# Optimization experiments

Hardware: AMD Instinct MI355X
Metric: run time of the kernel (lower is better)

Reference implementation:

```python
import jax, jax.numpy as jnp
import numpy as np

D_MODEL = 512
N_HEADS = 8
HEAD_DIM = D_MODEL // N_HEADS
NEG_INF = -1e9


def setup_inputs() -> dict:
    key = jax.random.key(0)
    ks = jax.random.split(key, 12)
    B, N, M = 8, 2048, 2048
    inp = {
        'query': jax.random.normal(ks[0], (B, D_MODEL, N), jnp.float32),
        'key': jax.random.normal(ks[1], (B, D_MODEL, M), jnp.float32),
        'value': jax.random.normal(ks[2], (B, D_MODEL, M), jnp.float32),
        'query_mask': jnp.ones((B, N), jnp.float32),
        'key_value_mask': jnp.ones((B, M), jnp.float32),
        # Conv1d(d_model, d_model, kernel_size=1) == pointwise linear: W [out, in], b [out]
        'Wq': jax.random.normal(ks[3], (D_MODEL, D_MODEL), jnp.float32) / np.sqrt(D_MODEL),
        'bq': jax.random.normal(ks[4], (D_MODEL,), jnp.float32) * 0.01,
        'Wk': jax.random.normal(ks[5], (D_MODEL, D_MODEL), jnp.float32) / np.sqrt(D_MODEL),
        'bk': jax.random.normal(ks[6], (D_MODEL,), jnp.float32) * 0.01,
        'Wv': jax.random.normal(ks[7], (D_MODEL, D_MODEL), jnp.float32) / np.sqrt(D_MODEL),
        'bv': jax.random.normal(ks[8], (D_MODEL,), jnp.float32) * 0.01,
        'Wm': jax.random.normal(ks[9], (D_MODEL, D_MODEL), jnp.float32) / np.sqrt(D_MODEL),
        'bm': jax.random.normal(ks[10], (D_MODEL,), jnp.float32) * 0.01,
    }
    return inp


def _pointwise(W, b, x):
    # Conv1d k=1 over [B, C_in, N] -> [B, C_out, N]
    return jnp.einsum('oi,bin->bon', W, x) + b[None, :, None]


def reference(query, key, value, query_mask, key_value_mask,
              Wq, bq, Wk, bk, Wv, bv, Wm, bm):
    B = query.shape[0]
    N = query.shape[2]
    M = key.shape[2]
    # project and split heads: [B, head_dim, n_heads, seq]
    q = _pointwise(Wq, bq, query).reshape(B, HEAD_DIM, N_HEADS, N)
    k = _pointwise(Wk, bk, key).reshape(B, HEAD_DIM, N_HEADS, M)
    v = _pointwise(Wv, bv, value).reshape(B, HEAD_DIM, N_HEADS, M)
    # scores [B, H, N, M], scaled by sqrt(head_dim) (query.shape[1] post-split)
    scores = jnp.einsum('bdhn,bdhm->bhnm', q, k) / jnp.sqrt(jnp.float32(HEAD_DIM))
    # dual mask: outer product of key_value_mask [B,1,1,M] and query_mask [B,1,N,1]
    mask = key_value_mask[:, None, None, :] * query_mask[:, None, :, None]
    scores = jnp.where(mask > 0, scores, NEG_INF)
    prob = jax.nn.softmax(scores, axis=-1)  # [B, H, N, M]
    x = jnp.einsum('bhnm,bdhm->bdhn', prob, v)  # [B, head_dim, H, N]
    out = _pointwise(Wm, bm, x.reshape(B, D_MODEL, N))
    return out
```

## Files before the change

### kernel.cpp

```cpp
#include <hip/hip_runtime.h>


typedef _Float16 f16;
typedef _Float16 f16x4 __attribute__((ext_vector_type(4)));
typedef _Float16 f16x8 __attribute__((ext_vector_type(8)));
typedef float f32x4 __attribute__((ext_vector_type(4)));

#define D_MODEL 512
#define HD 64
#define SEQ 2048
#define QSCL 0.18033688011112042f
#define KVNEG -1.4426950409e9f
#define FMAXB -6.0f

__global__ __launch_bounds__(256) void k_transpose(
    const float* __restrict__ q, const float* __restrict__ k, const float* __restrict__ v,
    f16* __restrict__ XT)
{
  __shared__ __align__(16) f16 Ts[64][72];
  int t = threadIdx.x;
  int nt = blockIdx.x, ct = blockIdx.y, z = blockIdx.z;
  int src = z >> 3, b = z & 7;
  const float* S = (src == 0) ? q : (src == 1) ? k : v;
  {
    int cr = t >> 2, ns = t & 3;
    const float* p = S + ((size_t)b * D_MODEL + ct * 64 + cr) * SEQ + nt * 64 + ns * 16;
    f32x4 a0 = *(const f32x4*)(p);
    f32x4 a1 = *(const f32x4*)(p + 4);
    f32x4 a2 = *(const f32x4*)(p + 8);
    f32x4 a3 = *(const f32x4*)(p + 12);
    f16x8 h0, h1;
#pragma unroll
    for (int j = 0; j < 4; ++j) { h0[j] = (f16)a0[j]; h0[4 + j] = (f16)a1[j]; h1[j] = (f16)a2[j]; h1[4 + j] = (f16)a3[j]; }
    *(f16x8*)&Ts[cr][ns * 16] = h0;
    *(f16x8*)&Ts[cr][ns * 16 + 8] = h1;
  }
  __syncthreads();
  {
    int nr = t >> 2, cs = t & 3;
    f16x8 h0, h1;
#pragma unroll
    for (int j = 0; j < 8; ++j) h0[j] = Ts[cs * 16 + j][nr];
#pragma unroll
    for (int j = 0; j < 8; ++j) h1[j] = Ts[cs * 16 + 8 + j][nr];
    f16* dst = XT + (((size_t)z) * SEQ + nt * 64 + nr) * D_MODEL + ct * 64 + cs * 16;
    *(f16x8*)dst = h0;
    *(f16x8*)(dst + 8) = h1;
  }
}

__global__ __launch_bounds__(256) void k_wconv(
    const float* __restrict__ Wq, const float* __restrict__ Wk, const float* __restrict__ Wv,
    const float* __restrict__ Wm, f16* __restrict__ W3, f16* __restrict__ Wmh)
{
  int idx = blockIdx.x * 256 + threadIdx.x;
  if (idx < 262144) {
    W3[idx] = (f16)Wq[idx];
    W3[262144 + idx] = (f16)Wk[idx];
    W3[524288 + idx] = (f16)Wv[idx];
    int o = idx >> 9, c = idx & 511;
    int h = c & 7, d = c >> 3;
    Wmh[((size_t)h * 512 + o) * 64 + d] = (f16)Wm[idx];
  }
}

__global__ __launch_bounds__(256, 2) void k_proj(
    const f16* __restrict__ W3, const float* __restrict__ bq, const float* __restrict__ bk,
    const float* __restrict__ bv, const f16* __restrict__ XT,
    f16* __restrict__ Qt, f16* __restrict__ Kt, f16* __restrict__ Vh)
{
  __shared__ __align__(16) char smem[36864];
  f16 (*As)[72] = (f16(*)[72])smem;
  f16 (*Bs)[72] = (f16(*)[72])(smem + 18432);
  f16 (*Ls)[136] = (f16(*)[136])smem;

  int t = threadIdx.x;
  int proj = blockIdx.z, b = blockIdx.y;
  int ot = blockIdx.x & 3, ntile = blockIdx.x >> 2;
  int w = t >> 6, ln = t & 63, i16 = ln & 15, q4 = ln >> 4;
  int ow = w >> 1, nw = w & 1;

  const f16* Wp = W3 + (size_t)proj * 262144;
  const f16* Xp = XT + ((size_t)proj * 8 + b) * (size_t)SEQ * D_MODEL;

  f32x4 acc[4][4];
#pragma unroll
  for (int x = 0; x < 4; ++x)
#pragma unroll
    for (int y = 0; y < 4; ++y) acc[x][y] = (f32x4){0.f, 0.f, 0.f, 0.f};

  int srow = t >> 1, shalf = t & 1;
  for (int kc = 0; kc < 8; ++kc) {
    __syncthreads();
    const f16* Ap = Wp + ((size_t)(ot * 128 + srow)) * 512 + kc * 64 + shalf * 32;
#pragma unroll
    for (int s8 = 0; s8 < 4; ++s8)
      *(f32x4*)&As[srow][shalf * 32 + s8 * 8] = *(const f32x4*)(Ap + s8 * 8);
    const f16* Bp = Xp + ((size_t)(ntile * 128 + srow)) * 512 + kc * 64 + shalf * 32;
#pragma unroll
    for (int s8 = 0; s8 < 4; ++s8)
      *(f32x4*)&Bs[srow][shalf * 32 + s8 * 8] = *(const f32x4*)(Bp + s8 * 8);
    __syncthreads();
#pragma unroll
    for (int kk = 0; kk < 2; ++kk) {
      f16x8 af[4], bf[4];
#pragma unroll
      for (int x = 0; x < 4; ++x) af[x] = *(const f16x8*)&As[ow * 64 + x * 16 + i16][kk * 32 + q4 * 8];
#pragma unroll
      for (int y = 0; y < 4; ++y) bf[y] = *(const f16x8*)&Bs[nw * 64 + y * 16 + i16][kk * 32 + q4 * 8];
#pragma unroll
      for (int x = 0; x < 4; ++x)
#pragma unroll
        for (int y = 0; y < 4; ++y)
          acc[x][y] = __builtin_amdgcn_mfma_f32_16x16x32_f16(af[x], bf[y], acc[x][y], 0, 0, 0);
    }
  }

  const float* bias = (proj == 0) ? bq : (proj == 1) ? bk : bv;
  float scl = (proj == 0) ? QSCL : 1.0f;
  __syncthreads();
#pragma unroll
  for (int x = 0; x < 4; ++x) {
    f32x4 bb = *(const f32x4*)(bias + ot * 128 + ow * 64 + x * 16 + q4 * 4);
#pragma unroll
    for (int y = 0; y < 4; ++y)
#pragma unroll
      for (int r = 0; r < 4; ++r)
        Ls[ow * 64 + x * 16 + q4 * 4 + r][nw * 64 + y * 16 + i16] = (f16)((acc[x][y][r] + bb[r]) * scl);
  }
  __syncthreads();
  if (proj < 2) {
    f16* dst = (proj == 0) ? Qt : Kt;
    int n = t >> 1, seg = t & 1;
#pragma unroll
    for (int h = 0; h < 8; ++h) {
      f16x8 g;
#pragma unroll
      for (int j = 0; j < 8; ++j) g[j] = Ls[8 * (seg * 8 + j) + h][n];
      f16* dp = dst + (((size_t)((b * 8 + h) * 4 + ot)) * 2048 + ntile * 128 + n) * 16 + seg * 8;
      *(f16x8*)dp = g;
    }
  } else {
#pragma unroll
    for (int p = 0; p < 8; ++p) {
      int ol = (t >> 4) + 16 * p;
      int ch = t & 15;
      int og = ot * 128 + ol;
      int h = og & 7, d = og >> 3;
      f16* dp = Vh + (((size_t)(b * 8 + h)) * HD + d) * SEQ + ntile * 128 + ch * 8;
      *(f32x4*)dp = *(const f32x4*)&Ls[ol][ch * 8];
    }
  }
}

__global__ __launch_bounds__(256, 4) void k_attn(
    const f16* __restrict__ Qt, const f16* __restrict__ Kt, const f16* __restrict__ Vh,
    const float* __restrict__ qmask, const float* __restrict__ kvmask,
    f16* __restrict__ O)
{
  __shared__ __align__(16) char smem[18432];
  f16 (*Qs)[72] = (f16(*)[72])smem;
  f16 (*Ks)[72] = (f16(*)[72])smem;
  f16 (*Vs)[72] = (f16(*)[72])(smem + 9216);

  int t = threadIdx.x;
  int bh = blockIdx.x >> 4;
  int b = bh >> 3;
  int n0 = (blockIdx.x & 15) * 128;
  int w = t >> 6, ln = t & 63, i16 = ln & 15, q4 = ln >> 4;

  const f16* Qb = Qt + (size_t)bh * 131072;
  const f16* Kb = Kt + (size_t)bh * 131072;
  const f16* Vb = Vh + (size_t)bh * HD * SEQ;
  const float* kvp = kvmask + (size_t)b * SEQ;

#pragma unroll
  for (int p = 0; p < 4; ++p) {
    int tid = p * 256 + t;
    int n = tid & 127, cx = tid >> 7;
    *(f32x4*)&Qs[n][cx * 8] =
        *(const f32x4*)(Qb + ((size_t)((cx >> 1) * 2048 + n0 + n)) * 16 + (cx & 1) * 8);
  }
  __syncthreads();
  f16x8 qf[2][2];
#pragma unroll
  for (int nt = 0; nt < 2; ++nt)
#pragma unroll
    for (int kc = 0; kc < 2; ++kc)
      qf[nt][kc] = *(const f16x8*)&Qs[w * 32 + nt * 16 + i16][kc * 32 + q4 * 8];
#pragma unroll
  for (int nt = 0; nt < 2; ++nt) {
    float qok = qmask[(size_t)b * SEQ + n0 + w * 32 + nt * 16 + i16];
    f16 qz = (qok > 0.f) ? (f16)1 : (f16)0;
    qf[nt][0] *= qz;
    qf[nt][1] *= qz;
  }

  f32x4 acc_o[4][2];
#pragma unroll
  for (int dt = 0; dt < 4; ++dt)
#pragma unroll
    for (int nt = 0; nt < 2; ++nt) acc_o[dt][nt] = (f32x4){0.f, 0.f, 0.f, 0.f};
  float rsum2[2] = {0.f, 0.f};

  for (int it = 0; it < 32; ++it) {
    int m0 = it * 64;
    __syncthreads();
#pragma unroll
    for (int p = 0; p < 2; ++p) {
      int tid = p * 256 + t;
      int cx = tid >> 6, nk = tid & 63;
      *(f32x4*)&Ks[nk][cx * 8] =
          *(const f32x4*)(Kb + ((size_t)((cx >> 1) * 2048 + m0 + nk)) * 16 + (cx & 1) * 8);
      int vrow = tid >> 3, vch = tid & 7;
      *(f32x4*)&Vs[vrow][vch * 8] = *(const f32x4*)(Vb + (size_t)vrow * SEQ + m0 + vch * 8);
    }
    __syncthreads();

    f32x4 bias[4];
#pragma unroll
    for (int mt = 0; mt < 4; ++mt) {
      f32x4 kv = *(const f32x4*)(kvp + m0 + mt * 16 + q4 * 4);
#pragma unroll
      for (int r = 0; r < 4; ++r) bias[mt][r] = (kv[r] > 0.f) ? FMAXB : KVNEG;
    }

    f32x4 s[2][4];
#pragma unroll
    for (int mt = 0; mt < 4; ++mt) {
      f16x8 kf0 = *(const f16x8*)&Ks[mt * 16 + i16][q4 * 8];
      f16x8 kf1 = *(const f16x8*)&Ks[mt * 16 + i16][32 + q4 * 8];
      f32x4 a0 = __builtin_amdgcn_mfma_f32_16x16x32_f16(kf0, qf[0][0], bias[mt], 0, 0, 0);
      s[0][mt] = __builtin_amdgcn_mfma_f32_16x16x32_f16(kf1, qf[0][1], a0, 0, 0, 0);
      f32x4 a1 = __builtin_amdgcn_mfma_f32_16x16x32_f16(kf0, qf[1][0], bias[mt], 0, 0, 0);
      s[1][mt] = __builtin_amdgcn_mfma_f32_16x16x32_f16(kf1, qf[1][1], a1, 0, 0, 0);
    }

    f16x4 pf[4][2];
#pragma unroll
    for (int nt = 0; nt < 2; ++nt) {
      float rs = 0.f;
#pragma unroll
      for (int mt = 0; mt < 4; ++mt) {
        float p0 = __builtin_amdgcn_exp2f(s[nt][mt][0]);
        float p1 = __builtin_amdgcn_exp2f(s[nt][mt][1]);
        float p2 = __builtin_amdgcn_exp2f(s[nt][mt][2]);
        float p3 = __builtin_amdgcn_exp2f(s[nt][mt][3]);
        rs += (p0 + p1) + (p2 + p3);
        f16x4 pv;
        pv[0] = (f16)p0; pv[1] = (f16)p1; pv[2] = (f16)p2; pv[3] = (f16)p3;
        pf[mt][nt] = pv;
      }
      rsum2[nt] += rs;
    }

#pragma unroll
    for (int dt = 0; dt < 4; ++dt) {
      f16x4 vf[4];
#pragma unroll
      for (int mt = 0; mt < 4; ++mt)
        vf[mt] = *(const f16x4*)&Vs[dt * 16 + i16][mt * 16 + q4 * 4];
#pragma unroll
      for (int nt = 0; nt < 2; ++nt) {
        f32x4 o = acc_o[dt][nt];
#pragma unroll
        for (int mt = 0; mt < 4; ++mt)
          o = __builtin_amdgcn_mfma_f32_16x16x16f16(vf[mt], pf[mt][nt], o, 0, 0, 0);
        acc_o[dt][nt] = o;
      }
    }
  }

  __syncthreads();
  f16 (*Os)[72] = (f16(*)[72])(smem + w * 4608);
#pragma unroll
  for (int nt = 0; nt < 2; ++nt) {
    float l = rsum2[nt];
    l += __shfl_xor(l, 16, 64);
    l += __shfl_xor(l, 32, 64);
    float inv = 1.f / l;
#pragma unroll
    for (int dt = 0; dt < 4; ++dt) {
      f16x4 o4;
#pragma unroll
      for (int r = 0; r < 4; ++r) o4[r] = (f16)(acc_o[dt][nt][r] * inv);
      *(f16x4*)&Os[nt * 16 + i16][dt * 16 + q4 * 4] = o4;
    }
  }
  __syncthreads();
  f16* Ob = O + ((size_t)bh * SEQ + n0 + w * 32) * HD;
#pragma unroll
  for (int p = 0; p < 4; ++p) {
    int row = (ln >> 3) + 8 * p, ch = ln & 7;
    *(f32x4*)(Ob + (size_t)row * HD + ch * 8) = *(const f32x4*)&Os[row][ch * 8];
  }
}

__global__ __launch_bounds__(256, 2) void k_out(
    const f16* __restrict__ Wmh, const float* __restrict__ bm,
    const f16* __restrict__ O, float* __restrict__ out)
{
  __shared__ __align__(16) char smem[20480];
  f16 (*As)[40] = (f16(*)[40])smem;
  f16 (*Bs)[40] = (f16(*)[40])(smem + 10240);

  int t = threadIdx.x;
  int b = blockIdx.y;
  int ot = blockIdx.x & 3, ntile = blockIdx.x >> 2;
  int w = t >> 6, ln = t & 63, i16 = ln & 15, q4 = ln >> 4;
  int ow = w >> 1, nw = w & 1;

  f32x4 acc[4][4];
#pragma unroll
  for (int x = 0; x < 4; ++x)
#pragma unroll
    for (int y = 0; y < 4; ++y) acc[x][y] = (f32x4){0.f, 0.f, 0.f, 0.f};

  int srow = t >> 1, sseg = t & 1;
  for (int ck = 0; ck < 16; ++ck) {
    int h = ck >> 1, dc = ck & 1;
    __syncthreads();
    const f16* Ap = Wmh + ((size_t)h * 512 + ot * 128 + srow) * 64 + dc * 32 + sseg * 16;
    *(f32x4*)&As[srow][sseg * 16] = *(const f32x4*)(Ap);
    *(f32x4*)&As[srow][sseg * 16 + 8] = *(const f32x4*)(Ap + 8);
    const f16* Bp = O + (((size_t)(b * 8 + h)) * SEQ + ntile * 128 + srow) * 64 + dc * 32 + sseg * 16;
    *(f32x4*)&Bs[srow][sseg * 16] = *(const f32x4*)(Bp);
    *(f32x4*)&Bs[srow][sseg * 16 + 8] = *(const f32x4*)(Bp + 8);
    __syncthreads();
    f16x8 af[4], bf[4];
#pragma unroll
    for (int x = 0; x < 4; ++x) af[x] = *(const f16x8*)&As[ow * 64 + x * 16 + i16][q4 * 8];
#pragma unroll
    for (int y = 0; y < 4; ++y) bf[y] = *(const f16x8*)&Bs[nw * 64 + y * 16 + i16][q4 * 8];
#pragma unroll
    for (int x = 0; x < 4; ++x)
#pragma unroll
      for (int y = 0; y < 4; ++y)
        acc[x][y] = __builtin_amdgcn_mfma_f32_16x16x32_f16(af[x], bf[y], acc[x][y], 0, 0, 0);
  }

#pragma unroll
  for (int x = 0; x < 4; ++x) {
    f32x4 bb = *(const f32x4*)(bm + ot * 128 + ow * 64 + x * 16 + q4 * 4);
#pragma unroll
    for (int y = 0; y < 4; ++y)
#pragma unroll
      for (int r = 0; r < 4; ++r) {
        int o_g = ot * 128 + ow * 64 + x * 16 + q4 * 4 + r;
        int n_g = ntile * 128 + nw * 64 + y * 16 + i16;
        out[((size_t)b * 512 + o_g) * SEQ + n_g] = acc[x][y][r] + bb[r];
      }
  }
}

extern "C" void kernel_launch(void* const* d_in, const int* in_sizes, int n_in,
                              void* d_out, int out_size, void* d_ws, size_t ws_size,
                              hipStream_t stream)
{
  const float* query  = (const float*)d_in[0];
  const float* key    = (const float*)d_in[1];
  const float* value  = (const float*)d_in[2];
  const float* qmask  = (const float*)d_in[3];
  const float* kvmask = (const float*)d_in[4];
  const float* Wq = (const float*)d_in[5];
  const float* bq = (const float*)d_in[6];
  const float* Wk = (const float*)d_in[7];
  const float* bk = (const float*)d_in[8];
  const float* Wv = (const float*)d_in[9];
  const float* bv = (const float*)d_in[10];
  const float* Wm = (const float*)d_in[11];
  const float* bm = (const float*)d_in[12];
  float* out = (float*)d_out;

  char* ws = (char*)d_ws;
  f16* XT  = (f16*)(ws);
  f16* Qt  = (f16*)(ws + 50331648);
  f16* Kt  = (f16*)(ws + 67108864);
  f16* Vh  = (f16*)(ws + 83886080);
  f16* Oat = (f16*)(ws);
  f16* W3  = (f16*)(ws + 100663296);
  f16* Wmh = (f16*)(ws + 102236160);

  k_transpose<<<dim3(32, 8, 24), 256, 0, stream>>>(query, key, value, XT);
  k_wconv<<<1024, 256, 0, stream>>>(Wq, Wk, Wv, Wm, W3, Wmh);
  k_proj<<<dim3(64, 8, 3), 256, 0, stream>>>(W3, bq, bk, bv, XT, Qt, Kt, Vh);
  k_attn<<<1024, 256, 0, stream>>>(Qt, Kt, Vh, qmask, kvmask, Oat);
  k_out<<<dim3(64, 8), 256, 0, stream>>>(Wmh, bm, Oat, out);
}
```

Measured before the change: 331.7 us.

## Prefetch K/V tiles into registers and use 16x16x32 MFMA for PV

Global loads for the next K/V tile are issued into registers right after the barrier, so they overlap the current tile's compute instead of stalling before it. K rows are stored permuted in shared memory and the key-mask indexing is permuted to match, so the P fragments pack into f16x8 and the PV product can use the 16x16x32 MFMA, halving the MFMA instruction count there. s_setprio is raised around the MFMA sections to favour matrix issue across waves. The cost is extra register pressure from the prefetch buffers and more complex index permutation logic.

After: 329.2 us. Within noise of the previous version (-0.7%).

```diff
diff --git a/kernel.cpp b/kernel.cpp
--- a/kernel.cpp
+++ b/kernel.cpp
@@ -174,6 +174,23 @@
   const f16* Vb = Vh + (size_t)bh * HD * SEQ;
   const float* kvp = kvmask + (size_t)b * SEQ;
 
+  int tid0 = t, tid1 = 256 + t;
+  int cx0 = tid0 >> 6, nk0 = tid0 & 63;
+  int cx1 = tid1 >> 6, nk1 = tid1 & 63;
+  int rk0 = (nk0 & 32) | ((nk0 & 4) << 2) | ((nk0 >> 1) & 12) | (nk0 & 3);
+  int rk1 = (nk1 & 32) | ((nk1 & 4) << 2) | ((nk1 >> 1) & 12) | (nk1 & 3);
+  int vw0 = tid0 >> 3, vc0 = tid0 & 7;
+  int vw1 = tid1 >> 3, vc1 = tid1 & 7;
+  const f16* ksp0 = Kb + ((size_t)((cx0 >> 1) * 2048 + nk0)) * 16 + (cx0 & 1) * 8;
+  const f16* ksp1 = Kb + ((size_t)((cx1 >> 1) * 2048 + nk1)) * 16 + (cx1 & 1) * 8;
+  const f16* vsp0 = Vb + (size_t)vw0 * SEQ + vc0 * 8;
+  const f16* vsp1 = Vb + (size_t)vw1 * SEQ + vc1 * 8;
+
+  f32x4 kA = *(const f32x4*)(ksp0);
+  f32x4 kB = *(const f32x4*)(ksp1);
+  f32x4 vA = *(const f32x4*)(vsp0);
+  f32x4 vB = *(const f32x4*)(vsp1);
+
 #pragma unroll
   for (int p = 0; p < 4; ++p) {
     int tid = p * 256 + t;
@@ -206,26 +223,29 @@
   for (int it = 0; it < 32; ++it) {
     int m0 = it * 64;
     __syncthreads();
-#pragma unroll
-    for (int p = 0; p < 2; ++p) {
-      int tid = p * 256 + t;
-      int cx = tid >> 6, nk = tid & 63;
-      *(f32x4*)&Ks[nk][cx * 8] =
-          *(const f32x4*)(Kb + ((size_t)((cx >> 1) * 2048 + m0 + nk)) * 16 + (cx & 1) * 8);
-      int vrow = tid >> 3, vch = tid & 7;
-      *(f32x4*)&Vs[vrow][vch * 8] = *(const f32x4*)(Vb + (size_t)vrow * SEQ + m0 + vch * 8);
-    }
-    __syncthreads();
+    *(f32x4*)&Ks[rk0][cx0 * 8] = kA;
+    *(f32x4*)&Ks[rk1][cx1 * 8] = kB;
+    *(f32x4*)&Vs[vw0][vc0 * 8] = vA;
+    *(f32x4*)&Vs[vw1][vc1 * 8] = vB;
+    __syncthreads();
+    if (it < 31) {
+      int mo = (it + 1) * 64;
+      kA = *(const f32x4*)(ksp0 + (size_t)mo * 16);
+      kB = *(const f32x4*)(ksp1 + (size_t)mo * 16);
+      vA = *(const f32x4*)(vsp0 + mo);
+      vB = *(const f32x4*)(vsp1 + mo);
+    }
 
     f32x4 bias[4];
 #pragma unroll
     for (int mt = 0; mt < 4; ++mt) {
-      f32x4 kv = *(const f32x4*)(kvp + m0 + mt * 16 + q4 * 4);
+      f32x4 kv = *(const f32x4*)(kvp + m0 + ((mt >> 1) << 5) + ((mt & 1) << 2) + q4 * 8);
 #pragma unroll
       for (int r = 0; r < 4; ++r) bias[mt][r] = (kv[r] > 0.f) ? FMAXB : KVNEG;
     }
 
     f32x4 s[2][4];
+    __builtin_amdgcn_s_setprio(1);
 #pragma unroll
     for (int mt = 0; mt < 4; ++mt) {
       f16x8 kf0 = *(const f16x8*)&Ks[mt * 16 + i16][q4 * 8];
@@ -235,40 +255,42 @@
       f32x4 a1 = __builtin_amdgcn_mfma_f32_16x16x32_f16(kf0, qf[1][0], bias[mt], 0, 0, 0);
       s[1][mt] = __builtin_amdgcn_mfma_f32_16x16x32_f16(kf1, qf[1][1], a1, 0, 0, 0);
     }
-
-    f16x4 pf[4][2];
+    __builtin_amdgcn_s_setprio(0);
+
+    f16x8 pf[2][2];
 #pragma unroll
     for (int nt = 0; nt < 2; ++nt) {
       float rs = 0.f;
 #pragma unroll
-      for (int mt = 0; mt < 4; ++mt) {
-        float p0 = __builtin_amdgcn_exp2f(s[nt][mt][0]);
-        float p1 = __builtin_amdgcn_exp2f(s[nt][mt][1]);
-        float p2 = __builtin_amdgcn_exp2f(s[nt][mt][2]);
-        float p3 = __builtin_amdgcn_exp2f(s[nt][mt][3]);
-        rs += (p0 + p1) + (p2 + p3);
-        f16x4 pv;
-        pv[0] = (f16)p0; pv[1] = (f16)p1; pv[2] = (f16)p2; pv[3] = (f16)p3;
-        pf[mt][nt] = pv;
+      for (int mtp = 0; mtp < 2; ++mtp) {
+        f16x8 pv;
+#pragma unroll
+        for (int r = 0; r < 4; ++r) {
+          float p0 = __builtin_amdgcn_exp2f(s[nt][2 * mtp][r]);
+          float p1 = __builtin_amdgcn_exp2f(s[nt][2 * mtp + 1][r]);
+          rs += p0 + p1;
+          pv[r] = (f16)p0;
+          pv[4 + r] = (f16)p1;
+        }
+        pf[mtp][nt] = pv;
       }
       rsum2[nt] += rs;
     }
 
+    __builtin_amdgcn_s_setprio(1);
 #pragma unroll
     for (int dt = 0; dt < 4; ++dt) {
-      f16x4 vf[4];
-#pragma unroll
-      for (int mt = 0; mt < 4; ++mt)
-        vf[mt] = *(const f16x4*)&Vs[dt * 16 + i16][mt * 16 + q4 * 4];
+      f16x8 vf0 = *(const f16x8*)&Vs[dt * 16 + i16][q4 * 8];
+      f16x8 vf1 = *(const f16x8*)&Vs[dt * 16 + i16][32 + q4 * 8];
 #pragma unroll
       for (int nt = 0; nt < 2; ++nt) {
         f32x4 o = acc_o[dt][nt];
-#pragma unroll
-        for (int mt = 0; mt < 4; ++mt)
-          o = __builtin_amdgcn_mfma_f32_16x16x16f16(vf[mt], pf[mt][nt], o, 0, 0, 0);
+        o = __builtin_amdgcn_mfma_f32_16x16x32_f16(vf0, pf[0][nt], o, 0, 0, 0);
+        o = __builtin_amdgcn_mfma_f32_16x16x32_f16(vf1, pf[1][nt], o, 0, 0, 0);
         acc_o[dt][nt] = o;
       }
     }
+    __builtin_amdgcn_s_setprio(0);
   }
 
   __syncthreads();
```
